# Performance work log

Hardware: AMD Instinct MI355X
Metric: run time of the kernel (lower is better)

Reference implementation:

```python
import jax, jax.numpy as jnp
import numpy as np

D = 128  # head dim

def setup_inputs() -> dict:
    key = jax.random.key(0)
    k1, k2, k3, k4, k5 = jax.random.split(key, 5)
    B, N, M, C1, C2 = 4, 4096, 4096, 1024, 1024
    x = jax.random.normal(k1, (B, N, C1), dtype=jnp.float32)
    y = jax.random.normal(k2, (B, M, C2), dtype=jnp.float32)
    # Linear(c, d, bias=False): out = inp @ W where W is [c, d]
    Wq = jax.random.normal(k3, (C1, D), dtype=jnp.float32) / np.sqrt(C1)
    Wk = jax.random.normal(k4, (C2, D), dtype=jnp.float32) / np.sqrt(C2)
    Wv = jax.random.normal(k5, (C2, D), dtype=jnp.float32) / np.sqrt(C2)
    return {"x": x, "y": y, "Wq": Wq, "Wk": Wk, "Wv": Wv}

def reference(x, y, Wq, Wk, Wv):
    q = x @ Wq                               # [B, N, d]
    k = y @ Wk                               # [B, M, d]
    v = y @ Wv                               # [B, M, d]
    scale = 1.0 / jnp.sqrt(jnp.asarray(D, dtype=q.dtype))
    a = jnp.einsum('bnd,bmd->bnm', q, k) * scale
    a = jax.nn.softmax(a, axis=-1)           # softmax FIRST
    a = jnp.triu(a, k=1)                     # post-softmax causal mask (keeps strict upper)
    out = jnp.einsum('bnm,bmd->bnd', a, v)   # [B, N, d]
    return out
```

## Files before the change

kernel.cpp:

```cpp
#include <hip/hip_runtime.h>
#include <hip/hip_bf16.h>
#include <stdint.h>


typedef __attribute__((ext_vector_type(8))) __bf16    bf16x8;
typedef __attribute__((ext_vector_type(4))) float     floatx4;
typedef __attribute__((ext_vector_type(8))) uint16_t  u16x8;
typedef __attribute__((ext_vector_type(4))) uint32_t  u32x4;

#define DEVFN __device__ __forceinline__

DEVFN uint16_t f32_to_bf16(float f) {
  uint32_t u = __builtin_bit_cast(uint32_t, f);
  u += 0x7FFFu + ((u >> 16) & 1u);
  return (uint16_t)(u >> 16);
}

DEVFN uint32_t bcast(float f) { return __builtin_bit_cast(uint32_t, f); }

DEVFN uint32_t pack2_bf16(float a, float b) {
  return ((bcast(a) + 0x8000u) >> 16) | ((bcast(b) + 0x8000u) & 0xFFFF0000u);
}

DEVFN u32x4 pack_bf16_8(float4 a0, float4 a1) {
  u32x4 o;
  o[0] = pack2_bf16(a0.x, a0.y);
  o[1] = pack2_bf16(a0.z, a0.w);
  o[2] = pack2_bf16(a1.x, a1.y);
  o[3] = pack2_bf16(a1.z, a1.w);
  return o;
}

DEVFN void gl2lds16(const void* g, void* l) {
  __builtin_amdgcn_global_load_lds(
      (const __attribute__((address_space(1))) void*)g,
      (__attribute__((address_space(3))) void*)l, 16, 0, 0);
}

__global__ __launch_bounds__(256) void wt_kernel(
    const float* __restrict__ Wq, const float* __restrict__ Wk,
    const float* __restrict__ Wv, uint16_t* __restrict__ wt) {
  int tid = blockIdx.x * 256 + threadIdx.x;
  int mat = tid >> 14;
  int rem = tid & 16383;
  int n  = rem & 127;
  int k0 = rem >> 7;
  const float* W = (mat == 0) ? Wq : ((mat == 1) ? Wk : Wv);
  u16x8 v;
#pragma unroll
  for (int j = 0; j < 8; ++j) v[j] = f32_to_bf16(W[(k0 * 8 + j) * 128 + n]);
  *(u16x8*)&wt[mat * (128 * 1024) + n * 1024 + k0 * 8] = v;
}

__global__ __launch_bounds__(512, 4) void qkv_kernel(
    const float* __restrict__ x, const float* __restrict__ y,
    const uint16_t* __restrict__ wt, uint16_t* __restrict__ q,
    uint16_t* __restrict__ k, uint16_t* __restrict__ vt) {
  constexpr int LDT = 72;
  constexpr int ABUF = 128 * LDT;
  __shared__ __align__(16) uint16_t sA[2 * ABUF];
  __shared__ __align__(16) uint16_t sW[2 * ABUF];
  const int t = threadIdx.x;
  const int mat = blockIdx.y, rt = blockIdx.x;
  const float* A = (mat == 0) ? x : y;
  const uint16_t* Wt = wt + mat * (128 * 1024);
  const int lane = t & 63, wv = t >> 6;
  const int wr = wv >> 1, wc = wv & 1;
  const int cidx = lane & 15, quad = lane >> 4;
  const int sr = t >> 3;
  const int sc = (t & 7) * 8;
  const int Arow0 = rt * 128;

  floatx4 acc[2][4];
#pragma unroll
  for (int rg = 0; rg < 2; ++rg)
#pragma unroll
    for (int ng = 0; ng < 4; ++ng) acc[rg][ng] = (floatx4){0.f, 0.f, 0.f, 0.f};

  float4 a0r[2], a1r[2];
  u16x8 wfr[2];
#pragma unroll
  for (int u = 0; u < 2; ++u) {
    int row = u * 64 + sr;
    const float* ap = &A[(size_t)(Arow0 + row) * 1024 + sc];
    a0r[u] = *(const float4*)ap;
    a1r[u] = *(const float4*)(ap + 4);
    wfr[u] = *(const u16x8*)&Wt[row * 1024 + sc];
  }
#pragma unroll
  for (int u = 0; u < 2; ++u) {
    int row = u * 64 + sr;
    *(u32x4*)&sA[row * LDT + sc] = pack_bf16_8(a0r[u], a1r[u]);
    *(u16x8*)&sW[row * LDT + sc] = wfr[u];
  }
  __syncthreads();

  for (int kt = 0; kt < 16; ++kt) {
    const int cur = kt & 1, nxt = cur ^ 1;
    if (kt < 15) {
      const int kc = (kt + 1) * 64;
#pragma unroll
      for (int u = 0; u < 2; ++u) {
        int row = u * 64 + sr;
        const float* ap = &A[(size_t)(Arow0 + row) * 1024 + kc + sc];
        a0r[u] = *(const float4*)ap;
        a1r[u] = *(const float4*)(ap + 4);
        wfr[u] = *(const u16x8*)&Wt[row * 1024 + kc + sc];
      }
    }
    bf16x8 af[2][2];
#pragma unroll
    for (int rg = 0; rg < 2; ++rg)
#pragma unroll
      for (int ks = 0; ks < 2; ++ks)
        af[rg][ks] = *(const bf16x8*)
            &sA[cur * ABUF + (wr * 32 + rg * 16 + cidx) * LDT + ks * 32 + quad * 8];
#pragma unroll
    for (int ng = 0; ng < 4; ++ng) {
      bf16x8 b0 = *(const bf16x8*)
          &sW[cur * ABUF + (wc * 64 + ng * 16 + cidx) * LDT + quad * 8];
      bf16x8 b1 = *(const bf16x8*)
          &sW[cur * ABUF + (wc * 64 + ng * 16 + cidx) * LDT + 32 + quad * 8];
#pragma unroll
      for (int rg = 0; rg < 2; ++rg) {
        acc[rg][ng] = __builtin_amdgcn_mfma_f32_16x16x32_bf16(af[rg][0], b0, acc[rg][ng], 0, 0, 0);
        acc[rg][ng] = __builtin_amdgcn_mfma_f32_16x16x32_bf16(af[rg][1], b1, acc[rg][ng], 0, 0, 0);
      }
    }
    if (kt < 15) {
#pragma unroll
      for (int u = 0; u < 2; ++u) {
        int row = u * 64 + sr;
        *(u32x4*)&sA[nxt * ABUF + row * LDT + sc] = pack_bf16_8(a0r[u], a1r[u]);
        *(u16x8*)&sW[nxt * ABUF + row * LDT + sc] = wfr[u];
      }
    }
    __syncthreads();
  }

  if (mat < 2) {
    uint16_t* outp = (mat == 0) ? q : k;
#pragma unroll
    for (int rg = 0; rg < 2; ++rg)
#pragma unroll
      for (int r = 0; r < 4; ++r) {
        int row = Arow0 + wr * 32 + rg * 16 + quad * 4 + r;
#pragma unroll
        for (int ng = 0; ng < 4; ++ng)
          outp[row * 128 + wc * 64 + ng * 16 + cidx] = f32_to_bf16(acc[rg][ng][r]);
      }
  } else {
    int bq = rt >> 5;
    int mbase = (rt & 31) * 128;
#pragma unroll
    for (int rg = 0; rg < 2; ++rg)
#pragma unroll
      for (int r = 0; r < 4; ++r) {
        int m = mbase + wr * 32 + rg * 16 + quad * 4 + r;
#pragma unroll
        for (int ng = 0; ng < 4; ++ng)
          vt[(size_t)(bq * 128 + wc * 64 + ng * 16 + cidx) * 4096 + m] =
              f32_to_bf16(acc[rg][ng][r]);
      }
  }
}

__global__ __launch_bounds__(256, 2) void attn_kernel(
    const uint16_t* __restrict__ q, const uint16_t* __restrict__ k,
    const uint16_t* __restrict__ vt, float* __restrict__ opart,
    float* __restrict__ lpart, int mlen, int iters) {
  constexpr int KB = 16384, VB = 16384;
  __shared__ __align__(16) uint8_t sK[2 * KB];
  __shared__ __align__(16) uint8_t sV[2 * VB];
  const int t = threadIdx.x;
  const int lane = t & 63, wv = t >> 6;
  const int cidx = lane & 15, quad = lane >> 4;
  const int qt = blockIdx.x, h = blockIdx.y, b = blockIdx.z;
  const int qmin = qt * 128 + wv * 32;
  const int mbase = h * mlen;

  const uint16_t* qb = q + (size_t)(b * 4096) * 128;
  const uint8_t* kb = (const uint8_t*)(k + (size_t)(b * 4096) * 128);
  const uint8_t* vb = (const uint8_t*)(vt + (size_t)(b * 128) * 4096);

  const float SC = 0.12751744610657223f;

  int kOffL[4], vOffL[4], kLds[4], vLds[4];
#pragma unroll
  for (int u = 0; u < 4; ++u) {
    int r  = wv * 16 + u * 4 + (lane >> 4);
    int g  = (lane & 15) ^ (r & 15);
    kOffL[u] = r * 256 + g * 16;
    kLds[u]  = (wv * 16 + u * 4) * 256;
    int rv = wv * 32 + u * 8 + (lane >> 3);
    int gv = (lane & 7) ^ (rv & 7);
    vOffL[u] = rv * 8192 + gv * 16;
    vLds[u]  = (wv * 32 + u * 8) * 128;
  }

  bf16x8 qf[2][4];
#pragma unroll
  for (int qg = 0; qg < 2; ++qg)
#pragma unroll
    for (int ks = 0; ks < 4; ++ks)
      qf[qg][ks] = *(const bf16x8*)
          &qb[(qmin + qg * 16 + cidx) * 128 + ks * 32 + quad * 8];

  floatx4 O[2][8];
#pragma unroll
  for (int qg = 0; qg < 2; ++qg)
#pragma unroll
    for (int dg = 0; dg < 8; ++dg) O[qg][dg] = (floatx4){0.f, 0.f, 0.f, 0.f};
  float lsum[2] = {0.f, 0.f};

#pragma unroll
  for (int u = 0; u < 4; ++u) {
    gl2lds16(kb + (size_t)mbase * 256 + kOffL[u], sK + kLds[u]);
    gl2lds16(vb + (size_t)mbase * 2 + vOffL[u], sV + vLds[u]);
  }
  __syncthreads();

  for (int it = 0; it < iters; ++it) {
    const int m0 = mbase + it * 64;
    const int cur = it & 1, nxt = cur ^ 1;
    if (it + 1 < iters) {
      const int m1 = m0 + 64;
#pragma unroll
      for (int u = 0; u < 4; ++u) {
        gl2lds16(kb + (size_t)m1 * 256 + kOffL[u], sK + nxt * KB + kLds[u]);
        gl2lds16(vb + (size_t)m1 * 2 + vOffL[u], sV + nxt * VB + vLds[u]);
      }
    }

    floatx4 accST[2][4];
#pragma unroll
    for (int qg = 0; qg < 2; ++qg)
#pragma unroll
      for (int ng = 0; ng < 4; ++ng) accST[qg][ng] = (floatx4){0.f, 0.f, 0.f, 0.f};
#pragma unroll
    for (int ks = 0; ks < 4; ++ks)
#pragma unroll
      for (int ng = 0; ng < 4; ++ng) {
        bf16x8 kf = *(const bf16x8*)
            (sK + cur * KB + (ng * 16 + cidx) * 256 + ((ks * 4 + quad) ^ cidx) * 16);
        accST[0][ng] = __builtin_amdgcn_mfma_f32_16x16x32_bf16(kf, qf[0][ks], accST[0][ng], 0, 0, 0);
        accST[1][ng] = __builtin_amdgcn_mfma_f32_16x16x32_bf16(kf, qf[1][ks], accST[1][ng], 0, 0, 0);
      }

    float p[2][4][4];
#pragma unroll
    for (int qg = 0; qg < 2; ++qg)
#pragma unroll
      for (int ng = 0; ng < 4; ++ng)
#pragma unroll
        for (int r = 0; r < 4; ++r) {
          p[qg][ng][r] = exp2f(accST[qg][ng][r] * SC);
          lsum[qg] += p[qg][ng][r];
        }

    if (m0 + 63 > qmin) {
#pragma unroll
      for (int qg = 0; qg < 2; ++qg) {
        const int base = qmin + qg * 16;
        if (m0 < base + 16) {
#pragma unroll
          for (int ng = 0; ng < 4; ++ng)
#pragma unroll
            for (int r = 0; r < 4; ++r) {
              int m = m0 + ng * 16 + quad * 4 + r;
              int n = base + cidx;
              if (m <= n) p[qg][ng][r] = 0.f;
            }
        }
      }
      uint32_t pk[2][4][2];
#pragma unroll
      for (int qg = 0; qg < 2; ++qg)
#pragma unroll
        for (int ng = 0; ng < 4; ++ng) {
          pk[qg][ng][0] = pack2_bf16(p[qg][ng][0], p[qg][ng][1]);
          pk[qg][ng][1] = pack2_bf16(p[qg][ng][2], p[qg][ng][3]);
        }
#pragma unroll
      for (int ks = 0; ks < 2; ++ks) {
        bf16x8 pbv[2];
#pragma unroll
        for (int qg = 0; qg < 2; ++qg) {
          u32x4 pbw;
#pragma unroll
          for (int j2 = 0; j2 < 4; ++j2) {
            int lr = ((quad & 1) << 3) + 2 * j2;
            int srcl = ((lr >> 2) << 4) + cidx;
            uint32_t lo = (uint32_t)__shfl((int)pk[qg][2 * ks][j2 & 1], srcl);
            uint32_t hi = (uint32_t)__shfl((int)pk[qg][2 * ks + 1][j2 & 1], srcl);
            pbw[j2] = (quad & 2) ? hi : lo;
          }
          pbv[qg] = __builtin_bit_cast(bf16x8, pbw);
        }
#pragma unroll
        for (int dg = 0; dg < 8; ++dg) {
          bf16x8 vf = *(const bf16x8*)
              (sV + cur * VB + (dg * 16 + cidx) * 128 +
               (((ks * 4 + quad) ^ cidx) & 7) * 16);
          O[0][dg] = __builtin_amdgcn_mfma_f32_16x16x32_bf16(vf, pbv[0], O[0][dg], 0, 0, 0);
          O[1][dg] = __builtin_amdgcn_mfma_f32_16x16x32_bf16(vf, pbv[1], O[1][dg], 0, 0, 0);
        }
      }
    }
    __syncthreads();
  }

#pragma unroll
  for (int qg = 0; qg < 2; ++qg) {
    lsum[qg] += __shfl_xor(lsum[qg], 16);
    lsum[qg] += __shfl_xor(lsum[qg], 32);
    const int n = qmin + qg * 16 + cidx;
    float* op = opart + ((size_t)h * 16384 + b * 4096 + n) * 128;
#pragma unroll
    for (int dg = 0; dg < 8; ++dg)
      *(float4*)&op[dg * 16 + quad * 4] = __builtin_bit_cast(float4, O[qg][dg]);
    if (quad == 0) lpart[h * 16384 + b * 4096 + n] = lsum[qg];
  }
}

__global__ __launch_bounds__(256) void combine_kernel(
    const float* __restrict__ opart, const float* __restrict__ lpart,
    float* __restrict__ out, int hcount) {
  size_t i = (size_t)blockIdx.x * 256 + threadIdx.x;
  size_t e = i * 4;
  int row = (int)(e >> 7);
  float4 acc = {0.f, 0.f, 0.f, 0.f};
  float l = 0.f;
  for (int h = 0; h < hcount; ++h) {
    float4 ov = *(const float4*)&opart[(size_t)h * 2097152 + e];
    acc.x += ov.x; acc.y += ov.y; acc.z += ov.z; acc.w += ov.w;
    l += lpart[h * 16384 + row];
  }
  float inv = 1.0f / l;
  float4 o;
  o.x = acc.x * inv; o.y = acc.y * inv; o.z = acc.z * inv; o.w = acc.w * inv;
  *(float4*)&out[e] = o;
}

extern "C" void kernel_launch(void* const* d_in, const int* in_sizes, int n_in,
                              void* d_out, int out_size, void* d_ws, size_t ws_size,
                              hipStream_t stream) {
  const float* x  = (const float*)d_in[0];
  const float* y  = (const float*)d_in[1];
  const float* Wq = (const float*)d_in[2];
  const float* Wk = (const float*)d_in[3];
  const float* Wv = (const float*)d_in[4];
  uint16_t* ws = (uint16_t*)d_ws;
  uint16_t* wt = ws;
  uint16_t* q  = ws + 393216;
  uint16_t* k  = q + 2097152;
  uint16_t* vt = k + 2097152;
  float* opart = (float*)((char*)d_ws + 13369344);
  int hcount = (ws_size >= (size_t)13369344 + 4 * 8454144) ? 4 : 2;
  float* lpart = opart + (size_t)hcount * 2097152;
  float* o = (float*)d_out;
  int mlen = 4096 / hcount, iters = mlen / 64;

  hipLaunchKernelGGL(wt_kernel,      dim3(192),            dim3(256), 0, stream, Wq, Wk, Wv, wt);
  hipLaunchKernelGGL(qkv_kernel,     dim3(128, 3),         dim3(512), 0, stream, x, y, wt, q, k, vt);
  hipLaunchKernelGGL(attn_kernel,    dim3(32, hcount, 4),  dim3(256), 0, stream, q, k, vt, opart, lpart, mlen, iters);
  hipLaunchKernelGGL(combine_kernel, dim3(2048),           dim3(256), 0, stream, opart, lpart, o, hcount);
}
```

Baseline: 235.3 us.

## Stage QKV weights via direct global-to-LDS loads with XOR-swizzled shared layout

In the QKV projection GEMM, weight tiles now go straight from global memory to LDS through an async copy helper instead of passing through registers. Both shared buffers drop the padded row stride for a 128-byte row layout with an XOR swizzle, to avoid bank conflicts without wasting LDS. The activation prefetch is reorganised, and the pipeline now uses explicit vmcnt/lgkmcnt waits and raw barriers in place of __syncthreads. The aim is fewer VGPRs and instructions for staging and better overlap of loads with MFMA work. The cost is reliance on hand-placed wait counts, which must match the exact number of outstanding loads.

```diff
diff --git a/kernel.cpp b/kernel.cpp
--- a/kernel.cpp
+++ b/kernel.cpp
@@ -56,10 +56,9 @@
     const float* __restrict__ x, const float* __restrict__ y,
     const uint16_t* __restrict__ wt, uint16_t* __restrict__ q,
     uint16_t* __restrict__ k, uint16_t* __restrict__ vt) {
-  constexpr int LDT = 72;
-  constexpr int ABUF = 128 * LDT;
-  __shared__ __align__(16) uint16_t sA[2 * ABUF];
-  __shared__ __align__(16) uint16_t sW[2 * ABUF];
+  constexpr int TB = 16384;
+  __shared__ __align__(16) uint8_t sA[2 * TB];
+  __shared__ __align__(16) uint8_t sW[2 * TB];
   const int t = threadIdx.x;
   const int mat = blockIdx.y, rt = blockIdx.x;
   const float* A = (mat == 0) ? x : y;
@@ -67,75 +66,91 @@
   const int lane = t & 63, wv = t >> 6;
   const int wr = wv >> 1, wc = wv & 1;
   const int cidx = lane & 15, quad = lane >> 4;
-  const int sr = t >> 3;
-  const int sc = (t & 7) * 8;
   const int Arow0 = rt * 128;
 
+  const int ar  = t >> 2;
+  const int acq = t & 3;
+  const float* aptr = &A[(size_t)(Arow0 + ar) * 1024 + acq * 16];
+  const int aw0 = ar * 128 + (((2 * acq) ^ (ar & 7)) * 16);
+  const int aw1 = ar * 128 + (((2 * acq + 1) ^ (ar & 7)) * 16);
+
+  int wsrc[2], wdst[2];
+#pragma unroll
+  for (int i = 0; i < 2; ++i) {
+    int G = i * 512 + t;
+    int n = G >> 3, g = G & 7;
+    wsrc[i] = n * 1024 + ((g ^ (n & 7)) * 8);
+    wdst[i] = G * 16;
+  }
+
   floatx4 acc[2][4];
 #pragma unroll
   for (int rg = 0; rg < 2; ++rg)
 #pragma unroll
     for (int ng = 0; ng < 4; ++ng) acc[rg][ng] = (floatx4){0.f, 0.f, 0.f, 0.f};
 
-  float4 a0r[2], a1r[2];
-  u16x8 wfr[2];
-#pragma unroll
-  for (int u = 0; u < 2; ++u) {
-    int row = u * 64 + sr;
-    const float* ap = &A[(size_t)(Arow0 + row) * 1024 + sc];
-    a0r[u] = *(const float4*)ap;
-    a1r[u] = *(const float4*)(ap + 4);
-    wfr[u] = *(const u16x8*)&Wt[row * 1024 + sc];
-  }
-#pragma unroll
-  for (int u = 0; u < 2; ++u) {
-    int row = u * 64 + sr;
-    *(u32x4*)&sA[row * LDT + sc] = pack_bf16_8(a0r[u], a1r[u]);
-    *(u16x8*)&sW[row * LDT + sc] = wfr[u];
-  }
-  __syncthreads();
+  float4 f4[4], g4[4];
+
+#pragma unroll
+  for (int i = 0; i < 2; ++i)
+    gl2lds16(Wt + wsrc[i], sW + wdst[i]);
+#pragma unroll
+  for (int j = 0; j < 4; ++j) f4[j] = *(const float4*)(aptr + j * 4);
 
   for (int kt = 0; kt < 16; ++kt) {
     const int cur = kt & 1, nxt = cur ^ 1;
     if (kt < 15) {
       const int kc = (kt + 1) * 64;
 #pragma unroll
-      for (int u = 0; u < 2; ++u) {
-        int row = u * 64 + sr;
-        const float* ap = &A[(size_t)(Arow0 + row) * 1024 + kc + sc];
-        a0r[u] = *(const float4*)ap;
-        a1r[u] = *(const float4*)(ap + 4);
-        wfr[u] = *(const u16x8*)&Wt[row * 1024 + kc + sc];
-      }
-    }
+      for (int i = 0; i < 2; ++i)
+        gl2lds16(Wt + kc + wsrc[i], sW + nxt * TB + wdst[i]);
+#pragma unroll
+      for (int j = 0; j < 4; ++j) g4[j] = *(const float4*)(aptr + kc + j * 4);
+      __builtin_amdgcn_sched_barrier(0);
+      asm volatile("s_waitcnt vmcnt(6)" ::: "memory");
+    } else {
+      __builtin_amdgcn_sched_barrier(0);
+      asm volatile("s_waitcnt vmcnt(0)" ::: "memory");
+    }
+    __builtin_amdgcn_sched_barrier(0);
+
+    *(u32x4*)(sA + cur * TB + aw0) = pack_bf16_8(f4[0], f4[1]);
+    *(u32x4*)(sA + cur * TB + aw1) = pack_bf16_8(f4[2], f4[3]);
+    __builtin_amdgcn_sched_barrier(0);
+    asm volatile("s_waitcnt lgkmcnt(0)" ::: "memory");
+    __builtin_amdgcn_s_barrier();
+    __builtin_amdgcn_sched_barrier(0);
+
     bf16x8 af[2][2];
 #pragma unroll
     for (int rg = 0; rg < 2; ++rg)
 #pragma unroll
       for (int ks = 0; ks < 2; ++ks)
         af[rg][ks] = *(const bf16x8*)
-            &sA[cur * ABUF + (wr * 32 + rg * 16 + cidx) * LDT + ks * 32 + quad * 8];
+            (sA + cur * TB + (wr * 32 + rg * 16 + cidx) * 128 +
+             (((ks * 4 + quad) ^ (cidx & 7)) * 16));
 #pragma unroll
     for (int ng = 0; ng < 4; ++ng) {
+      const int n = wc * 64 + ng * 16 + cidx;
       bf16x8 b0 = *(const bf16x8*)
-          &sW[cur * ABUF + (wc * 64 + ng * 16 + cidx) * LDT + quad * 8];
+          (sW + cur * TB + n * 128 + (((quad) ^ (cidx & 7)) * 16));
       bf16x8 b1 = *(const bf16x8*)
-          &sW[cur * ABUF + (wc * 64 + ng * 16 + cidx) * LDT + 32 + quad * 8];
+          (sW + cur * TB + n * 128 + (((4 + quad) ^ (cidx & 7)) * 16));
 #pragma unroll
       for (int rg = 0; rg < 2; ++rg) {
         acc[rg][ng] = __builtin_amdgcn_mfma_f32_16x16x32_bf16(af[rg][0], b0, acc[rg][ng], 0, 0, 0);
         acc[rg][ng] = __builtin_amdgcn_mfma_f32_16x16x32_bf16(af[rg][1], b1, acc[rg][ng], 0, 0, 0);
       }
     }
+    __builtin_amdgcn_sched_barrier(0);
+    asm volatile("s_waitcnt lgkmcnt(0)" ::: "memory");
+    __builtin_amdgcn_s_barrier();
+    __builtin_amdgcn_sched_barrier(0);
+
     if (kt < 15) {
 #pragma unroll
-      for (int u = 0; u < 2; ++u) {
-        int row = u * 64 + sr;
-        *(u32x4*)&sA[nxt * ABUF + row * LDT + sc] = pack_bf16_8(a0r[u], a1r[u]);
-        *(u16x8*)&sW[nxt * ABUF + row * LDT + sc] = wfr[u];
-      }
-    }
-    __syncthreads();
+      for (int j = 0; j < 4; ++j) f4[j] = g4[j];
+    }
   }
 
   if (mat < 2) {
```

Result: no change. 230.9 us (-1.9%).
